# Kernel optimization log

Measured on AMD Instinct MI355X. Metric: run time of the kernel, lower is better.

Reference implementation:

```python
import jax, jax.numpy as jnp
import numpy as np

FEATURE_DIM = 768
LAMBDA_REG = 0.01
NUM_ITERS = 5
LR = 0.1
SIGMA = 2.0
MARGIN = 1.0
BN_EPS = 1e-5


def setup_inputs() -> dict:
    key = jax.random.key(0)
    ks = jax.random.split(key, 10)
    B, D = 32, FEATURE_DIM
    search_features = jax.random.normal(ks[0], (B, D, 32, 32), dtype=jnp.float32)
    target_features = jax.random.normal(ks[1], (B, D, 16, 16), dtype=jnp.float32)
    target_mask = jax.random.uniform(ks[2], (B, 1, 16, 16), dtype=jnp.float32)
    conv_w = jax.random.normal(ks[3], (D, D), dtype=jnp.float32) * (1.0 / np.sqrt(D))
    conv_b = jax.random.normal(ks[4], (D,), dtype=jnp.float32) * 0.01
    bn_gamma = jnp.ones((D,), dtype=jnp.float32)
    bn_beta = jnp.zeros((D,), dtype=jnp.float32)
    bn_mean = jax.random.normal(ks[5], (D,), dtype=jnp.float32) * 0.01
    bn_var = jax.random.uniform(ks[6], (D,), dtype=jnp.float32, minval=0.5, maxval=1.5)
    filter_init = jax.random.normal(ks[7], (1, D, 1, 1), dtype=jnp.float32) * 0.01
    return {
        "search_features": search_features,
        "target_features": target_features,
        "target_mask": target_mask,
        "conv_w": conv_w,
        "conv_b": conv_b,
        "bn_gamma": bn_gamma,
        "bn_beta": bn_beta,
        "bn_mean": bn_mean,
        "bn_var": bn_var,
        "filter_init": filter_init,
    }


def _proj(x, conv_w, conv_b, bn_gamma, bn_beta, bn_mean, bn_var):
    # 1x1 conv == channel-wise GEMM, then BatchNorm (eval mode, running stats)
    y = jnp.einsum('bdhw,ed->behw', x, conv_w) + conv_b[None, :, None, None]
    inv_std = bn_gamma / jnp.sqrt(bn_var + BN_EPS)
    return (y - bn_mean[None, :, None, None]) * inv_std[None, :, None, None] + bn_beta[None, :, None, None]


def _gaussian_label(mask):
    B, _, H, W = mask.shape
    yy, xx = jnp.meshgrid(jnp.arange(H, dtype=jnp.float32), jnp.arange(W, dtype=jnp.float32), indexing='ij')
    yy = yy[None, None]  # (1,1,H,W)
    xx = xx[None, None]
    msum = jnp.clip(mask.sum(axis=(2, 3), keepdims=True), 1.0)
    cy = (mask * yy).sum(axis=(2, 3), keepdims=True) / msum
    cx = (mask * xx).sum(axis=(2, 3), keepdims=True) / msum
    return jnp.exp(-((xx - cx) ** 2 + (yy - cy) ** 2) / (2.0 * SIGMA ** 2))


def reference(search_features, target_features, target_mask, conv_w, conv_b,
              bn_gamma, bn_beta, bn_mean, bn_var, filter_init):
    sp = _proj(search_features, conv_w, conv_b, bn_gamma, bn_beta, bn_mean, bn_var)
    tp = _proj(target_features, conv_w, conv_b, bn_gamma, bn_beta, bn_mean, bn_var)
    B = tp.shape[0]
    label = _gaussian_label(target_mask)  # (B,1,H',W')
    f = jnp.broadcast_to(filter_init, (B,) + filter_init.shape[1:])  # (B,D,1,1)
    for _ in range(NUM_ITERS):
        response = (tp * f).sum(axis=1, keepdims=True)  # (B,1,H',W')
        loss = jnp.maximum(MARGIN - response * label, 0.0)
        grad = jnp.where(loss > 0, -label * target_mask, 0.0)
        grad = grad.mean(axis=(2, 3), keepdims=True)  # (B,1,1,1), broadcasts over D
        f = f - LR * (grad + LAMBDA_REG * f)
    return (sp * f).sum(axis=1, keepdims=True)  # (B,1,H,W)
```

## Files before the change

kernel.cpp:

```cpp
#include <hip/hip_runtime.h>
#include <math.h>

#define DD   768
#define BB   32
#define NTP  256
#define NSP  1024
#define NT   (BB*NTP)
#define NS   (BB*NSP)
#define ECH  16
#define CHE  (DD/ECH)
#define NQ   4
#define QCH  (DD/NQ)

#define OFF_UP  0
#define OFF_VP  (OFF_UP + ECH*DD)
#define OFF_K   (OFF_VP + ECH*DD)
#define OFF_TR0 (OFF_K + 64)
#define OFF_TS0 (OFF_TR0 + NQ*NT)
#define OFF_SR  (OFF_TS0 + NQ*NT)
#define OFF_SS  (OFF_SR + NQ*NS)

#define A5 0.99500999000499900f

__global__ void k_prep(const float* __restrict__ w, const float* __restrict__ cb,
                       const float* __restrict__ gamma, const float* __restrict__ beta,
                       const float* __restrict__ mean, const float* __restrict__ var,
                       const float* __restrict__ fi, float* __restrict__ ws) {
    int bx = blockIdx.x;
    int t = threadIdx.x;
    if (bx < ECH) {
        __shared__ float wu[CHE], wv[CHE];
        if (t < CHE) {
            int e = bx * CHE + t;
            float inv = gamma[e] / sqrtf(var[e] + 1e-5f);
            wv[t] = inv;
            wu[t] = inv * fi[e];
        }
        __syncthreads();
        if (t < 192) {
            const float4* w4 = (const float4*)w;
            float4 Ru = {0,0,0,0}, Rv = {0,0,0,0};
            #pragma unroll
            for (int j = 0; j < CHE; ++j) {
                float4 x = w4[(size_t)(bx * CHE + j) * 192 + t];
                float a = wu[j], b = wv[j];
                Ru.x += x.x * a; Ru.y += x.y * a; Ru.z += x.z * a; Ru.w += x.w * a;
                Rv.x += x.x * b; Rv.y += x.y * b; Rv.z += x.z * b; Rv.w += x.w * b;
            }
            *(float4*)(ws + OFF_UP + bx * DD + t * 4) = Ru;
            *(float4*)(ws + OFF_VP + bx * DD + t * 4) = Rv;
        }
    } else {
        __shared__ float r1[256], r2[256];
        float a1 = 0.f, a2 = 0.f;
        for (int e = t; e < DD; e += 256) {
            float inv = gamma[e] / sqrtf(var[e] + 1e-5f);
            float x = (cb[e] - mean[e]) * inv + beta[e];
            a1 += x * fi[e];
            a2 += x;
        }
        r1[t] = a1; r2[t] = a2;
        __syncthreads();
        for (int s = 128; s > 0; s >>= 1) {
            if (t < s) { r1[t] += r1[t + s]; r2[t] += r2[t + s]; }
            __syncthreads();
        }
        if (t == 0) { ws[OFF_K] = r1[0]; ws[OFF_K + 1] = r2[0]; }
    }
}

__global__ __launch_bounds__(256, 8) void k_big(const float* __restrict__ sf,
                                                const float* __restrict__ tf,
                                                float* __restrict__ ws) {
    int bx = blockIdx.x;
    int t = threadIdx.x;
    int pxf4 = t & 31, sub = t >> 5;

    int b, q, cq; bool isS;
    if (bx < 1024) { isS = true;  cq = bx & 3; q = (bx >> 2) & 7; b = bx >> 5; }
    else           { isS = false; int u = bx - 1024; cq = u & 3; q = (u >> 2) & 1; b = u >> 3; }

    __shared__ float su[QCH], sv[QCH];
    if (t < QCH / 4) {
        float4 U = {0,0,0,0}, V = {0,0,0,0};
        #pragma unroll
        for (int ec = 0; ec < ECH; ++ec) {
            float4 a = ((const float4*)(ws + OFF_UP))[ec * 192 + cq * 48 + t];
            float4 c = ((const float4*)(ws + OFF_VP))[ec * 192 + cq * 48 + t];
            U.x += a.x; U.y += a.y; U.z += a.z; U.w += a.w;
            V.x += c.x; V.y += c.y; V.z += c.z; V.w += c.w;
        }
        ((float4*)su)[t] = U;
        ((float4*)sv)[t] = V;
    }
    __syncthreads();

    const float4* base;
    int STR;
    float4 *oR, *oS;
    if (isS) {
        base = (const float4*)sf + ((size_t)b * DD + cq * QCH + sub * 24) * (NSP/4) + q * 32 + pxf4;
        STR = NSP / 4;
        int g4 = b * 256 + q * 32 + pxf4;
        oR = (float4*)(ws + OFF_SR) + cq * (NS/4) + g4;
        oS = (float4*)(ws + OFF_SS) + cq * (NS/4) + g4;
    } else {
        base = (const float4*)tf + ((size_t)b * DD + cq * QCH + sub * 24) * (NTP/4) + q * 32 + pxf4;
        STR = NTP / 4;
        int g4 = b * 64 + q * 32 + pxf4;
        oR = (float4*)(ws + OFF_TR0) + cq * (NT/4) + g4;
        oS = (float4*)(ws + OFF_TS0) + cq * (NT/4) + g4;
    }

    int chb = sub * 24;
    float4 accR = {0,0,0,0}, accS = {0,0,0,0};
    float4 buf[6];
    #pragma unroll
    for (int k = 0; k < 6; ++k) buf[k] = base[(size_t)k * STR];
    #pragma unroll
    for (int i = 0; i < 24; ++i) {
        float4 v = buf[i % 6];
        if (i < 18) buf[i % 6] = base[(size_t)(i + 6) * STR];
        float u = su[chb + i], vb = sv[chb + i];
        accR.x += v.x * u;  accR.y += v.y * u;  accR.z += v.z * u;  accR.w += v.w * u;
        accS.x += v.x * vb; accS.y += v.y * vb; accS.z += v.z * vb; accS.w += v.w * vb;
    }

    __shared__ float4 redR[8][32], redS[8][32];
    redR[sub][pxf4] = accR; redS[sub][pxf4] = accS;
    __syncthreads();
    for (int s = 4; s > 0; s >>= 1) {
        if (sub < s) {
            float4 a = redR[sub + s][pxf4], m = redR[sub][pxf4];
            m.x += a.x; m.y += a.y; m.z += a.z; m.w += a.w; redR[sub][pxf4] = m;
            float4 c = redS[sub + s][pxf4], n = redS[sub][pxf4];
            n.x += c.x; n.y += c.y; n.z += c.z; n.w += c.w; redS[sub][pxf4] = n;
        }
        __syncthreads();
    }
    if (sub == 0) { *oR = redR[0][pxf4]; *oS = redS[0][pxf4]; }
}

__global__ void k_final(const float* __restrict__ mask, const float* __restrict__ ws,
                        float* __restrict__ out) {
    int b = blockIdx.x;
    int p = threadIdx.x;
    int lane = p & 63, wv = p >> 6;
    int h = p >> 4, w = p & 15;
    float K1 = ws[OFF_K], K2 = ws[OFF_K + 1];
    float r0 = K1, s0 = K2;
    #pragma unroll
    for (int cq = 0; cq < NQ; ++cq) {
        r0 += ws[OFF_TR0 + cq * NT + b * 256 + p];
        s0 += ws[OFF_TS0 + cq * NT + b * 256 + p];
    }
    float m = mask[b * 256 + p];
    __shared__ float cross[4];
    auto bsum = [&](float v) -> float {
        #pragma unroll
        for (int o = 32; o > 0; o >>= 1) v += __shfl_xor(v, o, 64);
        if (lane == 0) cross[wv] = v;
        __syncthreads();
        float r = cross[0] + cross[1] + cross[2] + cross[3];
        __syncthreads();
        return r;
    };
    float msum = bsum(m);
    float sy = bsum(m * (float)h);
    float sx = bsum(m * (float)w);
    msum = fmaxf(msum, 1.0f);
    float cy = sy / msum, cx = sx / msum;
    float dx = (float)w - cx, dy = (float)h - cy;
    float label = expf(-(dx * dx + dy * dy) * 0.125f);
    float A = 1.0f, c = 0.0f;
    const float decay = 1.0f - 0.1f * 0.01f;
    #pragma unroll
    for (int it = 0; it < 5; ++it) {
        float resp = A * r0 + c * s0;
        float gc = (1.0f - resp * label > 0.0f) ? (-label * m) : 0.0f;
        float g = bsum(gc) * (1.0f / 256.0f);
        c = decay * c - 0.1f * g;
        A *= decay;
    }
    int g4 = b * 256 + p;
    float4 R = {K1, K1, K1, K1}, S = {K2, K2, K2, K2};
    #pragma unroll
    for (int cq = 0; cq < NQ; ++cq) {
        float4 a = ((const float4*)(ws + OFF_SR))[cq * (NS/4) + g4];
        float4 d = ((const float4*)(ws + OFF_SS))[cq * (NS/4) + g4];
        R.x += a.x; R.y += a.y; R.z += a.z; R.w += a.w;
        S.x += d.x; S.y += d.y; S.z += d.z; S.w += d.w;
    }
    float4 o;
    o.x = A5 * R.x + c * S.x;
    o.y = A5 * R.y + c * S.y;
    o.z = A5 * R.z + c * S.z;
    o.w = A5 * R.w + c * S.w;
    ((float4*)out)[g4] = o;
}

extern "C" void kernel_launch(void* const* d_in, const int* in_sizes, int n_in,
                              void* d_out, int out_size, void* d_ws, size_t ws_size,
                              hipStream_t stream) {
    const float* sf    = (const float*)d_in[0];
    const float* tf    = (const float*)d_in[1];
    const float* mask  = (const float*)d_in[2];
    const float* w     = (const float*)d_in[3];
    const float* cb    = (const float*)d_in[4];
    const float* gamma = (const float*)d_in[5];
    const float* beta  = (const float*)d_in[6];
    const float* mean  = (const float*)d_in[7];
    const float* var   = (const float*)d_in[8];
    const float* fi    = (const float*)d_in[9];
    float* out = (float*)d_out;
    float* ws  = (float*)d_ws;

    k_prep <<<ECH + 1, 256, 0, stream>>>(w, cb, gamma, beta, mean, var, fi, ws);
    k_big  <<<1280,    256, 0, stream>>>(sf, tf, ws);
    k_final<<<BB,      256, 0, stream>>>(mask, ws, out);
}
```

Before: 36.59 us.

## Fuse final solver into main reduction kernel with atomic counter handoff

Merges the big projection-reduction kernel and the final filter-optimization kernel into one launch. Target blocks run first, write their per-pixel sums and bump a global counter; search blocks spin on that counter, redo the small per-batch filter iteration locally, and write output directly. Each block now reduces over all 768 channels (32 sub-groups, 8 float4 pixels) instead of a channel quarter, which removes the partial-sum workspace traffic and the third launch. The trade-offs are redundant per-block solver work, a spin-wait that relies on target blocks being scheduled first, and lower occupancy from the launch bound change.

```diff
diff --git a/kernel.cpp b/kernel.cpp
--- a/kernel.cpp
+++ b/kernel.cpp
@@ -9,16 +9,13 @@
 #define NS   (BB*NSP)
 #define ECH  16
 #define CHE  (DD/ECH)
-#define NQ   4
-#define QCH  (DD/NQ)
 
 #define OFF_UP  0
 #define OFF_VP  (OFF_UP + ECH*DD)
 #define OFF_K   (OFF_VP + ECH*DD)
-#define OFF_TR0 (OFF_K + 64)
-#define OFF_TS0 (OFF_TR0 + NQ*NT)
-#define OFF_SR  (OFF_TS0 + NQ*NT)
-#define OFF_SS  (OFF_SR + NQ*NS)
+#define OFF_CNT (OFF_K + 16)
+#define OFF_TR0 (OFF_CNT + 16)
+#define OFF_TS0 (OFF_TR0 + NT)
 
 #define A5 0.99500999000499900f
 
@@ -51,6 +48,7 @@
             *(float4*)(ws + OFF_VP + bx * DD + t * 4) = Rv;
         }
     } else {
+        if (t == 0) ((unsigned*)ws)[OFF_CNT] = 0u;
         __shared__ float r1[256], r2[256];
         float a1 = 0.f, a2 = 0.f;
         for (int e = t; e < DD; e += 256) {
@@ -69,24 +67,31 @@
     }
 }
 
-__global__ __launch_bounds__(256, 8) void k_big(const float* __restrict__ sf,
-                                                const float* __restrict__ tf,
-                                                float* __restrict__ ws) {
+__global__ __launch_bounds__(256, 5) void k_fused(const float* __restrict__ sf,
+                                                  const float* __restrict__ tf,
+                                                  const float* __restrict__ mask,
+                                                  float* __restrict__ ws,
+                                                  float* __restrict__ out) {
     int bx = blockIdx.x;
     int t = threadIdx.x;
-    int pxf4 = t & 31, sub = t >> 5;
-
-    int b, q, cq; bool isS;
-    if (bx < 1024) { isS = true;  cq = bx & 3; q = (bx >> 2) & 7; b = bx >> 5; }
-    else           { isS = false; int u = bx - 1024; cq = u & 3; q = (u >> 2) & 1; b = u >> 3; }
-
-    __shared__ float su[QCH], sv[QCH];
-    if (t < QCH / 4) {
+    int pxf4 = t & 7, sub = t >> 3;
+    bool isT = bx < 256;
+    int b, g;
+    if (isT) { b = bx >> 3; g = bx & 7; }
+    else     { int u = bx - 256; b = u >> 5; g = u & 31; }
+
+    const float4* base;
+    int STR;
+    if (isT) { base = (const float4*)tf + ((size_t)b * DD + sub * 24) * (NTP/4) + g * 8 + pxf4; STR = NTP/4; }
+    else     { base = (const float4*)sf + ((size_t)b * DD + sub * 24) * (NSP/4) + g * 8 + pxf4; STR = NSP/4; }
+
+    __shared__ float su[DD], sv[DD];
+    if (t < 192) {
         float4 U = {0,0,0,0}, V = {0,0,0,0};
         #pragma unroll
         for (int ec = 0; ec < ECH; ++ec) {
-            float4 a = ((const float4*)(ws + OFF_UP))[ec * 192 + cq * 48 + t];
-            float4 c = ((const float4*)(ws + OFF_VP))[ec * 192 + cq * 48 + t];
+            float4 a = ((const float4*)(ws + OFF_UP))[ec * 192 + t];
+            float4 c = ((const float4*)(ws + OFF_VP))[ec * 192 + t];
             U.x += a.x; U.y += a.y; U.z += a.z; U.w += a.w;
             V.x += c.x; V.y += c.y; V.z += c.z; V.w += c.w;
         }
@@ -94,23 +99,6 @@
         ((float4*)sv)[t] = V;
     }
     __syncthreads();
-
-    const float4* base;
-    int STR;
-    float4 *oR, *oS;
-    if (isS) {
-        base = (const float4*)sf + ((size_t)b * DD + cq * QCH + sub * 24) * (NSP/4) + q * 32 + pxf4;
-        STR = NSP / 4;
-        int g4 = b * 256 + q * 32 + pxf4;
-        oR = (float4*)(ws + OFF_SR) + cq * (NS/4) + g4;
-        oS = (float4*)(ws + OFF_SS) + cq * (NS/4) + g4;
-    } else {
-        base = (const float4*)tf + ((size_t)b * DD + cq * QCH + sub * 24) * (NTP/4) + q * 32 + pxf4;
-        STR = NTP / 4;
-        int g4 = b * 64 + q * 32 + pxf4;
-        oR = (float4*)(ws + OFF_TR0) + cq * (NT/4) + g4;
-        oS = (float4*)(ws + OFF_TS0) + cq * (NT/4) + g4;
-    }
 
     int chb = sub * 24;
     float4 accR = {0,0,0,0}, accS = {0,0,0,0};
@@ -126,10 +114,10 @@
         accS.x += v.x * vb; accS.y += v.y * vb; accS.z += v.z * vb; accS.w += v.w * vb;
     }
 
-    __shared__ float4 redR[8][32], redS[8][32];
+    __shared__ float4 redR[32][8], redS[32][8];
     redR[sub][pxf4] = accR; redS[sub][pxf4] = accS;
     __syncthreads();
-    for (int s = 4; s > 0; s >>= 1) {
+    for (int s = 16; s > 0; s >>= 1) {
         if (sub < s) {
             float4 a = redR[sub + s][pxf4], m = redR[sub][pxf4];
             m.x += a.x; m.y += a.y; m.z += a.z; m.w += a.w; redR[sub][pxf4] = m;
@@ -138,39 +126,56 @@
         }
         __syncthreads();
     }
-    if (sub == 0) { *oR = redR[0][pxf4]; *oS = redS[0][pxf4]; }
-}
-
-__global__ void k_final(const float* __restrict__ mask, const float* __restrict__ ws,
-                        float* __restrict__ out) {
-    int b = blockIdx.x;
-    int p = threadIdx.x;
-    int lane = p & 63, wv = p >> 6;
-    int h = p >> 4, w = p & 15;
+
+    if (isT) {
+        if (sub == 0) {
+            ((float4*)(ws + OFF_TR0))[b * 64 + g * 8 + pxf4] = redR[0][pxf4];
+            ((float4*)(ws + OFF_TS0))[b * 64 + g * 8 + pxf4] = redS[0][pxf4];
+        }
+        __syncthreads();
+        if (t == 0) {
+            __threadfence();
+            atomicAdd((unsigned*)ws + OFF_CNT, 1u);
+        }
+        return;
+    }
+
+    if (t == 0) {
+        unsigned c;
+        do {
+            c = __hip_atomic_load((unsigned*)ws + OFF_CNT, __ATOMIC_ACQUIRE,
+                                  __HIP_MEMORY_SCOPE_AGENT);
+            if (c < 256u) __builtin_amdgcn_s_sleep(16);
+        } while (c < 256u);
+    }
+    __syncthreads();
+
+    int p = t, lane = t & 63, wvi = t >> 6;
+    int hh = p >> 4, wp = p & 15;
     float K1 = ws[OFF_K], K2 = ws[OFF_K + 1];
-    float r0 = K1, s0 = K2;
-    #pragma unroll
-    for (int cq = 0; cq < NQ; ++cq) {
-        r0 += ws[OFF_TR0 + cq * NT + b * 256 + p];
-        s0 += ws[OFF_TS0 + cq * NT + b * 256 + p];
-    }
+    unsigned ru = __hip_atomic_load((const unsigned*)(ws + OFF_TR0) + b * 256 + p,
+                                    __ATOMIC_RELAXED, __HIP_MEMORY_SCOPE_AGENT);
+    unsigned su_ = __hip_atomic_load((const unsigned*)(ws + OFF_TS0) + b * 256 + p,
+                                     __ATOMIC_RELAXED, __HIP_MEMORY_SCOPE_AGENT);
+    float r0 = K1 + __uint_as_float(ru);
+    float s0 = K2 + __uint_as_float(su_);
     float m = mask[b * 256 + p];
     __shared__ float cross[4];
     auto bsum = [&](float v) -> float {
         #pragma unroll
         for (int o = 32; o > 0; o >>= 1) v += __shfl_xor(v, o, 64);
-        if (lane == 0) cross[wv] = v;
+        if (lane == 0) cross[wvi] = v;
         __syncthreads();
         float r = cross[0] + cross[1] + cross[2] + cross[3];
         __syncthreads();
         return r;
     };
     float msum = bsum(m);
-    float sy = bsum(m * (float)h);
-    float sx = bsum(m * (float)w);
+    float sy = bsum(m * (float)hh);
+    float sx = bsum(m * (float)wp);
     msum = fmaxf(msum, 1.0f);
     float cy = sy / msum, cx = sx / msum;
-    float dx = (float)w - cx, dy = (float)h - cy;
+    float dx = (float)wp - cx, dy = (float)hh - cy;
     float label = expf(-(dx * dx + dy * dy) * 0.125f);
     float A = 1.0f, c = 0.0f;
     const float decay = 1.0f - 0.1f * 0.01f;
@@ -178,25 +183,19 @@
     for (int it = 0; it < 5; ++it) {
         float resp = A * r0 + c * s0;
         float gc = (1.0f - resp * label > 0.0f) ? (-label * m) : 0.0f;
-        float g = bsum(gc) * (1.0f / 256.0f);
-        c = decay * c - 0.1f * g;
+        float gsum = bsum(gc) * (1.0f / 256.0f);
+        c = decay * c - 0.1f * gsum;
         A *= decay;
     }
-    int g4 = b * 256 + p;
-    float4 R = {K1, K1, K1, K1}, S = {K2, K2, K2, K2};
-    #pragma unroll
-    for (int cq = 0; cq < NQ; ++cq) {
-        float4 a = ((const float4*)(ws + OFF_SR))[cq * (NS/4) + g4];
-        float4 d = ((const float4*)(ws + OFF_SS))[cq * (NS/4) + g4];
-        R.x += a.x; R.y += a.y; R.z += a.z; R.w += a.w;
-        S.x += d.x; S.y += d.y; S.z += d.z; S.w += d.w;
-    }
-    float4 o;
-    o.x = A5 * R.x + c * S.x;
-    o.y = A5 * R.y + c * S.y;
-    o.z = A5 * R.z + c * S.z;
-    o.w = A5 * R.w + c * S.w;
-    ((float4*)out)[g4] = o;
+    if (t < 8) {
+        float4 R = redR[0][t], S = redS[0][t];
+        float4 o;
+        o.x = A5 * (K1 + R.x) + c * (K2 + S.x);
+        o.y = A5 * (K1 + R.y) + c * (K2 + S.y);
+        o.z = A5 * (K1 + R.z) + c * (K2 + S.z);
+        o.w = A5 * (K1 + R.w) + c * (K2 + S.w);
+        ((float4*)out)[b * 256 + g * 8 + t] = o;
+    }
 }
 
 extern "C" void kernel_launch(void* const* d_in, const int* in_sizes, int n_in,
@@ -216,6 +215,5 @@
     float* ws  = (float*)d_ws;
 
     k_prep <<<ECH + 1, 256, 0, stream>>>(w, cb, gamma, beta, mean, var, fi, ws);
-    k_big  <<<1280,    256, 0, stream>>>(sf, tf, ws);
-    k_final<<<BB,      256, 0, stream>>>(mask, ws, out);
+    k_fused<<<1280,    256, 0, stream>>>(sf, tf, mask, ws, out);
 }
```

Measured after the change: 58.05 us. +58.6%, slower.

## Stage k_big input tiles into LDS via async global_load_lds double buffering

Applied to the files above, without the earlier changes.

Replaces the per-thread register prefetch of six float4 channel rows with a double-buffered LDS pipeline. Each 16-channel tile is fetched through `__builtin_amdgcn_global_load_lds`, with a block barrier after every tile. The reduction scratch now reuses the staging buffers, and the min-blocks launch bound is dropped. The aim is to overlap global loads with the FMA work and cut register pressure. The risk is less memory parallelism: only one 8KB tile per block is in flight, there are 12 barriers per block, and the kernel depends on the compiler inserting the right waits for the async LDS loads.

```diff
diff --git a/kernel.cpp b/kernel.cpp
--- a/kernel.cpp
+++ b/kernel.cpp
@@ -11,6 +11,8 @@
 #define CHE  (DD/ECH)
 #define NQ   4
 #define QCH  (DD/NQ)
+#define BUFCH 16
+#define NBUF  (QCH/BUFCH)
 
 #define OFF_UP  0
 #define OFF_VP  (OFF_UP + ECH*DD)
@@ -21,6 +23,9 @@
 #define OFF_SS  (OFF_SR + NQ*NS)
 
 #define A5 0.99500999000499900f
+
+typedef __attribute__((address_space(1))) const void glb_cvoid;
+typedef __attribute__((address_space(3))) void lds_void;
 
 __global__ void k_prep(const float* __restrict__ w, const float* __restrict__ cb,
                        const float* __restrict__ gamma, const float* __restrict__ beta,
@@ -69,18 +74,21 @@
     }
 }
 
-__global__ __launch_bounds__(256, 8) void k_big(const float* __restrict__ sf,
-                                                const float* __restrict__ tf,
-                                                float* __restrict__ ws) {
+__global__ __launch_bounds__(256) void k_big(const float* __restrict__ sf,
+                                             const float* __restrict__ tf,
+                                             float* __restrict__ ws) {
     int bx = blockIdx.x;
     int t = threadIdx.x;
     int pxf4 = t & 31, sub = t >> 5;
+    int wv_ = t >> 6, ln = t & 63;
 
     int b, q, cq; bool isS;
     if (bx < 1024) { isS = true;  cq = bx & 3; q = (bx >> 2) & 7; b = bx >> 5; }
     else           { isS = false; int u = bx - 1024; cq = u & 3; q = (u >> 2) & 1; b = u >> 3; }
 
+    __shared__ float4 stage[2][BUFCH * 32];
     __shared__ float su[QCH], sv[QCH];
+
     if (t < QCH / 4) {
         float4 U = {0,0,0,0}, V = {0,0,0,0};
         #pragma unroll
@@ -93,52 +101,71 @@
         ((float4*)su)[t] = U;
         ((float4*)sv)[t] = V;
     }
-    __syncthreads();
 
     const float4* base;
     int STR;
     float4 *oR, *oS;
     if (isS) {
-        base = (const float4*)sf + ((size_t)b * DD + cq * QCH + sub * 24) * (NSP/4) + q * 32 + pxf4;
+        base = (const float4*)sf + ((size_t)b * DD + cq * QCH) * (NSP/4) + q * 32;
         STR = NSP / 4;
         int g4 = b * 256 + q * 32 + pxf4;
         oR = (float4*)(ws + OFF_SR) + cq * (NS/4) + g4;
         oS = (float4*)(ws + OFF_SS) + cq * (NS/4) + g4;
     } else {
-        base = (const float4*)tf + ((size_t)b * DD + cq * QCH + sub * 24) * (NTP/4) + q * 32 + pxf4;
+        base = (const float4*)tf + ((size_t)b * DD + cq * QCH) * (NTP/4) + q * 32;
         STR = NTP / 4;
         int g4 = b * 64 + q * 32 + pxf4;
         oR = (float4*)(ws + OFF_TR0) + cq * (NT/4) + g4;
         oS = (float4*)(ws + OFF_TS0) + cq * (NT/4) + g4;
     }
 
-    int chb = sub * 24;
+    auto STAGE = [&](int bi, int cblk) {
+        #pragma unroll
+        for (int j = 0; j < 2; ++j) {
+            int inst = wv_ * 2 + j;
+            int f = inst * 64 + ln;
+            int ch = f >> 5, p4 = f & 31;
+            const float4* g = base + (size_t)(cblk * BUFCH + ch) * STR + p4;
+            float4* lp = &stage[bi][inst * 64];
+            __builtin_amdgcn_global_load_lds((glb_cvoid*)g, (lds_void*)lp, 16, 0, 0);
+        }
+    };
+
+    STAGE(0, 0);
+    __syncthreads();
+
     float4 accR = {0,0,0,0}, accS = {0,0,0,0};
-    float4 buf[6];
-    #pragma unroll
-    for (int k = 0; k < 6; ++k) buf[k] = base[(size_t)k * STR];
-    #pragma unroll
-    for (int i = 0; i < 24; ++i) {
-        float4 v = buf[i % 6];
-        if (i < 18) buf[i % 6] = base[(size_t)(i + 6) * STR];
-        float u = su[chb + i], vb = sv[chb + i];
-        accR.x += v.x * u;  accR.y += v.y * u;  accR.z += v.z * u;  accR.w += v.w * u;
-        accS.x += v.x * vb; accS.y += v.y * vb; accS.z += v.z * vb; accS.w += v.w * vb;
-    }
-
-    __shared__ float4 redR[8][32], redS[8][32];
-    redR[sub][pxf4] = accR; redS[sub][pxf4] = accS;
+    int cur = 0;
+    #pragma unroll
+    for (int cblk = 0; cblk < NBUF; ++cblk) {
+        if (cblk < NBUF - 1) STAGE(cur ^ 1, cblk + 1);
+        #pragma unroll
+        for (int i = 0; i < 2; ++i) {
+            int chl = sub * 2 + i;
+            float4 v = stage[cur][chl * 32 + pxf4];
+            float u = su[cblk * BUFCH + chl], vb = sv[cblk * BUFCH + chl];
+            accR.x += v.x * u;  accR.y += v.y * u;  accR.z += v.z * u;  accR.w += v.w * u;
+            accS.x += v.x * vb; accS.y += v.y * vb; accS.z += v.z * vb; accS.w += v.w * vb;
+        }
+        __syncthreads();
+        cur ^= 1;
+    }
+
+    float4* redR = (float4*)&stage[0][0];
+    float4* redS = (float4*)&stage[1][0];
+    redR[sub * 32 + pxf4] = accR;
+    redS[sub * 32 + pxf4] = accS;
     __syncthreads();
     for (int s = 4; s > 0; s >>= 1) {
         if (sub < s) {
-            float4 a = redR[sub + s][pxf4], m = redR[sub][pxf4];
-            m.x += a.x; m.y += a.y; m.z += a.z; m.w += a.w; redR[sub][pxf4] = m;
-            float4 c = redS[sub + s][pxf4], n = redS[sub][pxf4];
-            n.x += c.x; n.y += c.y; n.z += c.z; n.w += c.w; redS[sub][pxf4] = n;
-        }
-        __syncthreads();
-    }
-    if (sub == 0) { *oR = redR[0][pxf4]; *oS = redS[0][pxf4]; }
+            float4 a = redR[(sub + s) * 32 + pxf4], m = redR[sub * 32 + pxf4];
+            m.x += a.x; m.y += a.y; m.z += a.z; m.w += a.w; redR[sub * 32 + pxf4] = m;
+            float4 c = redS[(sub + s) * 32 + pxf4], n = redS[sub * 32 + pxf4];
+            n.x += c.x; n.y += c.y; n.z += c.z; n.w += c.w; redS[sub * 32 + pxf4] = n;
+        }
+        __syncthreads();
+    }
+    if (sub == 0) { *oR = redR[pxf4]; *oS = redS[pxf4]; }
 }
 
 __global__ void k_final(const float* __restrict__ mask, const float* __restrict__ ws,
```

Result: faster. 34.81 us (-4.9%).
